# Performance work log

Hardware: AMD Instinct MI355X
Metric: run time of the kernel (lower is better)

Reference implementation:

```python
import jax, jax.numpy as jnp
import numpy as np

K = 4096          # num_embeddings
D = 256           # embedding_dim
BETA = 0.25
DECAY = 0.99
EPS = 1e-05

def setup_inputs() -> dict:
    key = jax.random.key(0)
    k1, k2, k3 = jax.random.split(key, 3)
    N = 65536
    return {
        "z": jax.random.normal(k1, (N, D), dtype=jnp.float32),
        "weight": jax.random.normal(k2, (K, D), dtype=jnp.float32),
        "ema_w": jax.random.normal(k3, (K, D), dtype=jnp.float32),
        "ema_cluster_size": jnp.ones((K,), dtype=jnp.float32),
    }

def reference(z, weight, ema_w, ema_cluster_size):
    # pairwise squared distances: [N, K]
    d = (jnp.sum(z * z, axis=1, keepdims=True)
         + jnp.sum(weight * weight, axis=1)
         - 2.0 * jnp.matmul(z, weight.T))
    idx = jnp.argmin(d, axis=1)                     # [N]
    encodings = jax.nn.one_hot(idx, K, dtype=z.dtype)  # [N, K]

    # EMA codebook update (training branch). In torch the results are re-wrapped
    # into fresh nn.Parameters, which detaches them from the autograd graph.
    def _ema(z_, enc_, ema_w_, cs_):
        cs = cs_ * DECAY + (1.0 - DECAY) * jnp.sum(enc_, axis=0)
        n = jnp.sum(cs)
        cs = (cs + EPS) / (n + K * EPS) * n
        dw = jnp.matmul(enc_.T, z_)                 # [K, D] scatter-add of z by code
        new_ema_w = ema_w_ * DECAY + (1.0 - DECAY) * dw
        new_weight = new_ema_w / cs[:, None]
        return cs, new_ema_w, new_weight
    new_cs, new_ema_w, new_weight = jax.lax.stop_gradient(
        _ema(z, encodings, ema_w, ema_cluster_size))

    z_q = new_weight[idx]                           # [N, D] gather from updated codebook
    loss = (jnp.mean((jax.lax.stop_gradient(z_q) - z) ** 2)
            + BETA * jnp.mean((z_q - jax.lax.stop_gradient(z)) ** 2))
    avg_probs = jnp.mean(encodings, axis=0)
    perplexity = jnp.exp(-jnp.sum(avg_probs * jnp.log(avg_probs + 1e-10)))
    z_q = z + jax.lax.stop_gradient(z_q - z)        # straight-through estimator
    return (z_q, idx[:, None], loss, perplexity, new_cs, new_ema_w, new_weight)
```

## Files before the change

### kernel.cpp

```cpp
#include <hip/hip_runtime.h>
#include <math.h>

#define NPTS 65536
#define DIMD 256
#define KCB  4096
#define MARGIN 2.0f

#define O_ZQ   0
#define O_IDX  16777216
#define O_LOSS 16842752
#define O_PERP 16842753
#define O_CS   16842754
#define O_EMAW 16846850
#define O_W    17895426

#define OFF_WSW   8388608
#define OFF_CCNT  8912896
#define OFF_CIDS  8978432
#define OFF_OFFS  10027008
#define OFF_CUR   10031232
#define OFF_ROWS  10035328
#define OFF_GMIN  10100864
#define OFF_CHOF  10166400
#define OFF_BMIN  10240000
#define OFF_RL    11288576
#define OFF_TPRE  12338176

#define CHK 64
#define MAXCHUNKS 5120
#define PADL 65600

#define RING 6
#define PFD  4

typedef __attribute__((ext_vector_type(8))) short short8;
typedef __attribute__((ext_vector_type(4))) float f32x4;

__device__ __forceinline__ unsigned short f2bf(float f) {
    unsigned u = __float_as_uint(f);
    return (unsigned short)((u + 0x7FFF + ((u >> 16) & 1)) >> 16);
}
__device__ __forceinline__ unsigned encf(float f) {
    unsigned u = __float_as_uint(f);
    return (u >> 31) ? ~u : (u | 0x80000000u);
}
__device__ __forceinline__ float decf(unsigned e) {
    unsigned u = (e & 0x80000000u) ? (e & 0x7fffffffu) : ~e;
    return __uint_as_float(u);
}

__global__ void k_prepz(const float* __restrict__ src, unsigned* __restrict__ dst,
                        float* __restrict__ ss) {
    int l   = threadIdx.x & 63;
    int row = blockIdx.x * 4 + (threadIdx.x >> 6);
    float4 v = ((const float4*)(src + (size_t)row * DIMD))[l];
    uint2 pk = make_uint2(f2bf(v.x) | (f2bf(v.y) << 16),
                          f2bf(v.z) | (f2bf(v.w) << 16));
    ((uint2*)dst)[(size_t)row * 64 + l] = pk;
    float s = v.x*v.x + v.y*v.y + v.z*v.z + v.w*v.w;
    #pragma unroll
    for (int off = 32; off; off >>= 1) s += __shfl_down(s, off);
    if (l == 0) ss[row] = s;
}

__global__ void k_prepw(const float* __restrict__ src, unsigned* __restrict__ dst,
                        float* __restrict__ ss) {
    int l   = threadIdx.x & 63;
    int row = blockIdx.x * 4 + (threadIdx.x >> 6);
    float4 v = ((const float4*)(src + (size_t)row * DIMD))[l];
    uint2 pk = make_uint2(f2bf(v.x) | (f2bf(v.y) << 16),
                          f2bf(v.z) | (f2bf(v.w) << 16));
    int g = row >> 4, n16 = row & 15;
    int c = l >> 3, q = (l >> 1) & 3, half = l & 1;
    ((uint2*)dst)[g * 1024 + c * 128 + (q * 16 + n16) * 2 + half] = pk;
    float s = v.x*v.x + v.y*v.y + v.z*v.z + v.w*v.w;
    #pragma unroll
    for (int off = 32; off; off >>= 1) s += __shfl_down(s, off);
    if (l == 0) ss[row] = s;
}

__launch_bounds__(256, 2)
__global__ void k_pass0(const unsigned* __restrict__ zbf,
                        const uint4* __restrict__ wsw4,
                        const float* __restrict__ wwg,
                        unsigned* __restrict__ gmin,
                        float* __restrict__ bmin) {
    __shared__ __align__(16) char smem[RING * 8192];
    __shared__ float lds_ww[2048];
    const int t = threadIdx.x, wv = t >> 6, l = t & 63;
    const int q = l >> 4, n16 = l & 15;
    const int rb    = blockIdx.x >> 1;
    const int half  = blockIdx.x & 1;
    const int row0  = rb * 256 + wv * 64;
    const int g0    = half * 128;
    const int ph0   = (blockIdx.x * 48) & 127;

    union U { uint4 u; short8 s; } afr[4][8];
    #pragma unroll
    for (int s = 0; s < 4; ++s) {
        const char* zb = (const char*)zbf + ((size_t)(row0 + s * 16 + n16) << 9) + q * 16;
        #pragma unroll
        for (int c = 0; c < 8; ++c) afr[s][c].u = *(const uint4*)(zb + c * 64);
    }

    auto stage = [&](int buf, int g) {
        const int ga = (ph0 + g) & 127;
        const uint4* srcb = wsw4 + (size_t)(g0 + ga) * 512;
        #pragma unroll
        for (int j = 0; j < 2; ++j) {
            int rrow = j * 4 + wv;
            __builtin_amdgcn_global_load_lds(
                (const __attribute__((address_space(1))) unsigned*)(srcb + rrow * 64 + l),
                (__attribute__((address_space(3))) unsigned*)(&smem[buf * 8192 + rrow * 1024]),
                16, 0, 0);
        }
    };

    for (int i = t; i < 2048; i += 256) lds_ww[i] = wwg[g0 * 16 + i];
    #pragma unroll
    for (int g = 0; g < PFD; ++g) stage(g, g);
    __syncthreads();

    float minv[16], bm[16];
    #pragma unroll
    for (int i = 0; i < 16; ++i) { minv[i] = 3.0e38f; bm[i] = 3.0e38f; }

    int buf = 0, sbuf = PFD;
    #pragma unroll 1
    for (int g = 0; g < 128; ++g) {
        if (g < 128 - PFD) {
            stage(sbuf, g + PFD);
            sbuf = (sbuf == RING - 1) ? 0 : sbuf + 1;
            asm volatile("s_waitcnt vmcnt(8)" ::: "memory");
        } else {
            asm volatile("s_waitcnt vmcnt(0)" ::: "memory");
        }
        __builtin_amdgcn_s_barrier();
        const char* sbase = smem + buf * 8192;
        buf = (buf == RING - 1) ? 0 : buf + 1;
        const int ga = (ph0 + g) & 127;
        f32x4 acc[4];
        #pragma unroll
        for (int s = 0; s < 4; ++s) acc[s] = (f32x4){0.f, 0.f, 0.f, 0.f};
        __builtin_amdgcn_s_setprio(1);
        #pragma unroll
        for (int c = 0; c < 8; ++c) {
            U bf; bf.u = *(const uint4*)(sbase + c * 1024 + (l << 4));
            #pragma unroll
            for (int s = 0; s < 4; ++s)
                acc[s] = __builtin_amdgcn_mfma_f32_16x16x32_bf16(afr[s][c].s, bf.s, acc[s], 0, 0, 0);
        }
        __builtin_amdgcn_s_setprio(0);
        float wwv = lds_ww[ga * 16 + n16];
        #pragma unroll
        for (int s = 0; s < 4; ++s)
            #pragma unroll
            for (int r = 0; r < 4; ++r)
                bm[s*4+r] = fminf(bm[s*4+r], fmaf(-2.f, acc[s][r], wwv));
        if ((g & 15) == 15) {
            const int blk = (g0 + ((ph0 + (g & ~15)) & 127)) >> 4;
            #pragma unroll
            for (int i = 0; i < 16; ++i) {
                float m = bm[i];
                minv[i] = fminf(minv[i], m);
                #pragma unroll
                for (int msk = 1; msk < 16; msk <<= 1) m = fminf(m, __shfl_xor(m, msk));
                if (n16 == 0)
                    bmin[(size_t)(row0 + (i >> 2) * 16 + q * 4 + (i & 3)) * 16 + blk] = m;
                bm[i] = 3.0e38f;
            }
        }
    }

    #pragma unroll
    for (int i = 0; i < 16; ++i) {
        float m = minv[i];
        #pragma unroll
        for (int msk = 1; msk < 16; msk <<= 1) m = fminf(m, __shfl_xor(m, msk));
        if (n16 == 0)
            atomicMin(&gmin[row0 + (i >> 2) * 16 + q * 4 + (i & 3)], encf(m));
    }
}

__global__ void k_bsel(const unsigned* __restrict__ gmin,
                       const float* __restrict__ bmin,
                       int* __restrict__ bcnt, int* __restrict__ rlist) {
    __shared__ int lcnt[16], lbase[16], lcur[16];
    int t = threadIdx.x;
    if (t < 16) { lcnt[t] = 0; lcur[t] = 0; }
    __syncthreads();
    int row = blockIdx.x * 256 + t;
    float thr = decf(gmin[row]) + MARGIN;
    const float* bm = bmin + (size_t)row * 16;
    unsigned qual = 0;
    #pragma unroll
    for (int b = 0; b < 16; ++b)
        if (bm[b] <= thr) { qual |= (1u << b); atomicAdd(&lcnt[b], 1); }
    __syncthreads();
    if (t < 16) lbase[t] = atomicAdd(&bcnt[t], lcnt[t]);
    __syncthreads();
    #pragma unroll
    for (int b = 0; b < 16; ++b)
        if (qual & (1u << b)) {
            int p = atomicAdd(&lcur[b], 1);
            rlist[b * PADL + lbase[b] + p] = row;
        }
}

__global__ void k_btile(const int* __restrict__ bcnt, int* __restrict__ rlist,
                        int* __restrict__ tpre) {
    __shared__ int tb[16];
    int t = threadIdx.x;
    if (t < 16) tb[t] = (bcnt[t] + 63) >> 6;
    __syncthreads();
    int b = t >> 4, j = t & 15;
    int n = bcnt[b], e = tb[b] * 64;
    for (int i = n + j; i < e; i += 16) rlist[b * PADL + i] = -1;
    if (t == 0) {
        int s = 0;
        for (int b2 = 0; b2 < 16; ++b2) { tpre[b2] = s; s += tb[b2]; }
        tpre[16] = s;
    }
}

__launch_bounds__(256, 2)
__global__ void k_pass1(const unsigned* __restrict__ zbf,
                        const uint4* __restrict__ wsw4,
                        const float* __restrict__ wwg,
                        const unsigned* __restrict__ gmin,
                        const int* __restrict__ tpre,
                        const int* __restrict__ rlist,
                        int* __restrict__ ccnt,
                        int* __restrict__ cids) {
    const int t = threadIdx.x, wv = t >> 6, l = t & 63;
    const int q = l >> 4, n16 = l & 15;
    const int ntiles = tpre[16];
    for (int tile = blockIdx.x * 4 + wv; tile < ntiles; tile += 2048) {
        int b = 0;
        while (b < 15 && tpre[b + 1] <= tile) ++b;
        const int* rl = rlist + b * PADL + (tile - tpre[b]) * 64;

        union U { uint4 u; short8 s; } afr[4][8];
        #pragma unroll
        for (int s = 0; s < 4; ++s) {
            int r = rl[s * 16 + n16];
            int rr = r < 0 ? 0 : r;
            const char* zb = (const char*)zbf + ((size_t)rr << 9) + q * 16;
            #pragma unroll
            for (int c = 0; c < 8; ++c) afr[s][c].u = *(const uint4*)(zb + c * 64);
        }
        float thr[16];
        #pragma unroll
        for (int i = 0; i < 16; ++i) {
            int r = rl[(i >> 2) * 16 + q * 4 + (i & 3)];
            thr[i] = (r < 0) ? -3.0e38f : decf(gmin[r]) + MARGIN;
        }

        #pragma unroll 2
        for (int g = 0; g < 16; ++g) {
            const int gg = b * 16 + g;
            const uint4* wp = wsw4 + (size_t)gg * 512 + l;
            f32x4 acc[4];
            #pragma unroll
            for (int s = 0; s < 4; ++s) acc[s] = (f32x4){0.f, 0.f, 0.f, 0.f};
            #pragma unroll
            for (int c = 0; c < 8; ++c) {
                U bf; bf.u = wp[c * 64];
                #pragma unroll
                for (int s = 0; s < 4; ++s)
                    acc[s] = __builtin_amdgcn_mfma_f32_16x16x32_bf16(afr[s][c].s, bf.s, acc[s], 0, 0, 0);
            }
            float wwv = wwg[gg * 16 + n16];
            #pragma unroll
            for (int s = 0; s < 4; ++s)
                #pragma unroll
                for (int r = 0; r < 4; ++r) {
                    float core = fmaf(-2.f, acc[s][r], wwv);
                    if (core <= thr[s*4+r]) {
                        int row = rl[s * 16 + q * 4 + r];
                        int pos = atomicAdd(&ccnt[row], 1);
                        if (pos < 16) cids[row * 16 + pos] = gg * 16 + n16;
                    }
                }
        }
    }
}

__global__ void k_refine(const float* __restrict__ z,
                         const float* __restrict__ w,
                         const float* __restrict__ zz,
                         const float* __restrict__ wwg,
                         const int* __restrict__ ccnt,
                         const int* __restrict__ cids,
                         float* __restrict__ counts,
                         int*   __restrict__ idxi,
                         float* __restrict__ idxf) {
    int l   = threadIdx.x & 63;
    int row = blockIdx.x * 4 + (threadIdx.x >> 6);
    int n = ccnt[row]; if (n > 16) n = 16;
    float4 zv = ((const float4*)(z + (size_t)row * DIMD))[l];
    float zzv = zz[row];
    float bd = 3.0e38f; int bi = 0x7fffffff;
    for (int j = 0; j < n; ++j) {
        int k = cids[row * 16 + j];
        float4 wv = ((const float4*)(w + (size_t)k * DIMD))[l];
        float s = zv.x*wv.x + zv.y*wv.y + zv.z*wv.z + zv.w*wv.w;
        #pragma unroll
        for (int off = 32; off; off >>= 1) s += __shfl_xor(s, off);
        float d = (zzv + wwg[k]) - 2.0f * s;
        if (d < bd || (d == bd && k < bi)) { bd = d; bi = k; }
    }
    if (l == 0) {
        idxi[row] = bi;
        idxf[row] = (float)bi;
        atomicAdd(&counts[bi], 1.0f);
    }
}

__global__ void k_offsets(const float* __restrict__ counts,
                          int* __restrict__ offs, int* __restrict__ cursor,
                          int* __restrict__ choffs) {
    __shared__ int sc[1024];
    int t = threadIdx.x;
    int c[4]; int s = 0;
    #pragma unroll
    for (int i = 0; i < 4; ++i) { c[i] = (int)counts[t * 4 + i]; s += c[i]; }
    sc[t] = s;
    __syncthreads();
    for (int d = 1; d < 1024; d <<= 1) {
        int v = (t >= d) ? sc[t - d] : 0;
        __syncthreads();
        sc[t] += v;
        __syncthreads();
    }
    int o = sc[t] - s;
    #pragma unroll
    for (int i = 0; i < 4; ++i) { offs[t*4+i] = o; cursor[t*4+i] = o; o += c[i]; }
    if (t == 1023) offs[4096] = sc[1023];
    __syncthreads();

    int ch[4]; int s2 = 0;
    #pragma unroll
    for (int i = 0; i < 4; ++i) { ch[i] = (c[i] + CHK - 1) / CHK; s2 += ch[i]; }
    sc[t] = s2;
    __syncthreads();
    for (int d = 1; d < 1024; d <<= 1) {
        int v = (t >= d) ? sc[t - d] : 0;
        __syncthreads();
        sc[t] += v;
        __syncthreads();
    }
    int o2 = sc[t] - s2;
    #pragma unroll
    for (int i = 0; i < 4; ++i) { choffs[t*4+i] = o2; o2 += ch[i]; }
    if (t == 1023) choffs[4096] = sc[1023];
}

__global__ void k_fill(const int* __restrict__ idxi, int* __restrict__ cursor,
                       int* __restrict__ rows) {
    int r = blockIdx.x * 256 + threadIdx.x;
    int k = idxi[r];
    int pos = atomicAdd(&cursor[k], 1);
    rows[pos] = r;
}

__global__ void k_dw(const float* __restrict__ z, const int* __restrict__ offs,
                     const int* __restrict__ choffs, const int* __restrict__ rows,
                     float* __restrict__ dw) {
    __shared__ float4 part[4][64];
    int b = blockIdx.x;
    if (b >= choffs[KCB]) return;
    int lo = 0, hi = KCB;
    while (hi - lo > 1) { int mid = (lo + hi) >> 1; if (choffs[mid] <= b) lo = mid; else hi = mid; }
    int k  = lo;
    int ci = b - choffs[k];
    int o0 = offs[k] + ci * CHK;
    int o1 = offs[k + 1]; if (o1 > o0 + CHK) o1 = o0 + CHK;
    int l = threadIdx.x & 63, j = threadIdx.x >> 6;
    float4 a = make_float4(0.f, 0.f, 0.f, 0.f);
    for (int i = o0 + j; i < o1; i += 4) {
        int r = rows[i];
        float4 v = ((const float4*)(z + (size_t)r * DIMD))[l];
        a.x += v.x; a.y += v.y; a.z += v.z; a.w += v.w;
    }
    part[j][l] = a;
    __syncthreads();
    if (j == 0) {
        float4 bb = part[0][l], c = part[1][l], d = part[2][l], e = part[3][l];
        a = make_float4(bb.x+c.x+d.x+e.x, bb.y+c.y+d.y+e.y,
                        bb.z+c.z+d.z+e.z, bb.w+c.w+d.w+e.w);
        float* p = dw + (size_t)k * DIMD + l * 4;
        if (choffs[k + 1] - choffs[k] == 1) {
            *(float4*)p = a;
        } else {
            atomicAdd(p + 0, a.x); atomicAdd(p + 1, a.y);
            atomicAdd(p + 2, a.z); atomicAdd(p + 3, a.w);
        }
    }
}

__global__ void k_cs(const float* __restrict__ ema_cs,
                     float* __restrict__ cs_io,
                     float* __restrict__ perp) {
    __shared__ float2 red[16];
    int t = threadIdx.x;
    float csd[4];
    float nl = 0.f, el = 0.f;
    #pragma unroll
    for (int i = 0; i < 4; ++i) {
        int k = t * 4 + i;
        float c  = cs_io[k];
        float cd = ema_cs[k] * 0.99f + 0.01f * c;
        csd[i] = cd;
        nl += cd;
        float p = c * (1.0f / 65536.0f);
        el += p * logf(p + 1e-10f);
    }
    #pragma unroll
    for (int off = 32; off; off >>= 1) { nl += __shfl_down(nl, off); el += __shfl_down(el, off); }
    if ((t & 63) == 0) red[t >> 6] = make_float2(nl, el);
    __syncthreads();
    if (t == 0) {
        float n = 0.f, e = 0.f;
        for (int i = 0; i < 16; ++i) { n += red[i].x; e += red[i].y; }
        red[0] = make_float2(n, e);
        perp[0] = expf(-e);
    }
    __syncthreads();
    float n = red[0].x;
    float scale = n / (n + 4096.0f * 1e-5f);
    #pragma unroll
    for (int i = 0; i < 4; ++i)
        cs_io[t * 4 + i] = (csd[i] + 1e-5f) * scale;
}

__global__ void k_emaw(const float* __restrict__ ema_w,
                       const float* __restrict__ cs,
                       float* __restrict__ emaw_io,
                       float* __restrict__ wout) {
    int i = (blockIdx.x * 256 + threadIdx.x) * 4;
    int k = i >> 8;
    float4 dv = *(const float4*)(emaw_io + i);
    float4 ev = *(const float4*)(ema_w + i);
    float c = cs[k];
    float4 ne;
    ne.x = ev.x * 0.99f + 0.01f * dv.x;
    ne.y = ev.y * 0.99f + 0.01f * dv.y;
    ne.z = ev.z * 0.99f + 0.01f * dv.z;
    ne.w = ev.w * 0.99f + 0.01f * dv.w;
    *(float4*)(emaw_io + i) = ne;
    float4 nw = make_float4(ne.x / c, ne.y / c, ne.z / c, ne.w / c);
    *(float4*)(wout + i) = nw;
}

__global__ void k_zq(const float* __restrict__ z,
                     const float* __restrict__ wnew,
                     const int* __restrict__ idxi,
                     float* __restrict__ zq,
                     float* __restrict__ sqacc) {
    __shared__ float red[4];
    int i = (blockIdx.x * 256 + threadIdx.x) * 4;
    int n = i >> 8;
    int d = i & 255;
    int k = idxi[n];
    float4 wv = *(const float4*)(wnew + (k << 8) + d);
    float4 zv = *(const float4*)(z + i);
    float4 o;
    o.x = zv.x + (wv.x - zv.x);
    o.y = zv.y + (wv.y - zv.y);
    o.z = zv.z + (wv.z - zv.z);
    o.w = zv.w + (wv.w - zv.w);
    *(float4*)(zq + i) = o;
    float dx = wv.x - zv.x, dy = wv.y - zv.y, dz = wv.z - zv.z, dw_ = wv.w - zv.w;
    float s = dx*dx + dy*dy + dz*dz + dw_*dw_;
    #pragma unroll
    for (int off = 32; off; off >>= 1) s += __shfl_down(s, off);
    int lane = threadIdx.x & 63;
    if (lane == 0) red[threadIdx.x >> 6] = s;
    __syncthreads();
    if (threadIdx.x == 0)
        atomicAdd(&sqacc[blockIdx.x & 255], red[0] + red[1] + red[2] + red[3]);
}

__global__ void k_final(const float* __restrict__ sqacc, float* __restrict__ loss) {
    __shared__ float red[4];
    int t = threadIdx.x;
    float s = sqacc[t];
    #pragma unroll
    for (int off = 32; off; off >>= 1) s += __shfl_down(s, off);
    if ((t & 63) == 0) red[t >> 6] = s;
    __syncthreads();
    if (t == 0)
        loss[0] = 1.25f * (red[0] + red[1] + red[2] + red[3]) * (1.0f / 16777216.0f);
}

extern "C" void kernel_launch(void* const* d_in, const int* in_sizes, int n_in,
                              void* d_out, int out_size, void* d_ws, size_t ws_size,
                              hipStream_t stream) {
    const float* z      = (const float*)d_in[0];
    const float* weight = (const float*)d_in[1];
    const float* ema_w  = (const float*)d_in[2];
    const float* ema_cs = (const float*)d_in[3];
    float* out = (float*)d_out;
    float* ws  = (float*)d_ws;

    int*   bcnt = (int*)ws;
    float* scal = ws + 4096;
    int*   idxi = (int*)(ws + 8192);

    unsigned* zbf    = (unsigned*)(out + O_ZQ);
    uint4*    wsw4   = (uint4*)(out + O_ZQ + OFF_WSW);
    int*      ccnt   = (int*)(out + O_ZQ + OFF_CCNT);
    int*      cids   = (int*)(out + O_ZQ + OFF_CIDS);
    int*      offs   = (int*)(out + O_ZQ + OFF_OFFS);
    int*      cursor = (int*)(out + O_ZQ + OFF_CUR);
    int*      rows   = (int*)(out + O_ZQ + OFF_ROWS);
    unsigned* gmin   = (unsigned*)(out + O_ZQ + OFF_GMIN);
    int*      choffs = (int*)(out + O_ZQ + OFF_CHOF);
    float*    bmin   = out + O_ZQ + OFF_BMIN;
    int*      rlist  = (int*)(out + O_ZQ + OFF_RL);
    int*      tpre   = (int*)(out + O_ZQ + OFF_TPRE);
    float*    zz     = out + O_EMAW;
    float*    wwg    = out + O_EMAW + 65536;

    hipMemsetAsync(bcnt,       0,    16 * 4, stream);
    hipMemsetAsync(scal,       0,    256 * 4, stream);
    hipMemsetAsync(out + O_CS, 0,    (size_t)KCB * 4, stream);
    hipMemsetAsync(ccnt,       0,    (size_t)NPTS * 4, stream);
    hipMemsetAsync(gmin,       0xFF, (size_t)NPTS * 4, stream);

    k_prepz  <<<NPTS / 4, 256, 0, stream>>>(z, zbf, zz);
    k_prepw  <<<KCB  / 4, 256, 0, stream>>>(weight, (unsigned*)wsw4, wwg);
    k_pass0  <<<512, 256, 0, stream>>>(zbf, wsw4, wwg, gmin, bmin);
    k_bsel   <<<NPTS / 256, 256, 0, stream>>>(gmin, bmin, bcnt, rlist);
    k_btile  <<<1, 256, 0, stream>>>(bcnt, rlist, tpre);
    k_pass1  <<<512, 256, 0, stream>>>(zbf, wsw4, wwg, gmin, tpre, rlist,
                                       ccnt, cids);
    k_refine <<<NPTS / 4, 256, 0, stream>>>(z, weight, zz, wwg, ccnt, cids,
                                            out + O_CS, idxi, out + O_IDX);
    hipMemsetAsync(out + O_EMAW, 0, (size_t)KCB * DIMD * 4, stream);
    k_offsets<<<1, 1024, 0, stream>>>(out + O_CS, offs, cursor, choffs);
    k_fill   <<<NPTS / 256, 256, 0, stream>>>(idxi, cursor, rows);
    k_cs     <<<1, 1024, 0, stream>>>(ema_cs, out + O_CS, out + O_PERP);
    k_dw     <<<MAXCHUNKS, 256, 0, stream>>>(z, offs, choffs, rows, out + O_EMAW);
    k_emaw   <<<(KCB * DIMD) / 1024, 256, 0, stream>>>(ema_w, out + O_CS,
                                                       out + O_EMAW, out + O_W);
    k_zq     <<<(NPTS * DIMD) / 1024, 256, 0, stream>>>(z, out + O_W, idxi,
                                                        out + O_ZQ, scal);
    k_final  <<<1, 256, 0, stream>>>(scal, out + O_LOSS);
}
```

Before: 494.9 us.

## Fuse prep kernels, fold memsets into kernels, merge count stages, widen pass0 staging

```diff
diff --git a/kernel.cpp b/kernel.cpp
--- a/kernel.cpp
+++ b/kernel.cpp
@@ -24,14 +24,13 @@
 #define OFF_CHOF  10166400
 #define OFF_BMIN  10240000
 #define OFF_RL    11288576
-#define OFF_TPRE  12338176
 
 #define CHK 64
 #define MAXCHUNKS 5120
 #define PADL 65600
 
-#define RING 6
-#define PFD  4
+#define RING0 4
+#define NSLOT 64
 
 typedef __attribute__((ext_vector_type(8))) short short8;
 typedef __attribute__((ext_vector_type(4))) float f32x4;
@@ -49,34 +48,42 @@
     return __uint_as_float(u);
 }
 
-__global__ void k_prepz(const float* __restrict__ src, unsigned* __restrict__ dst,
-                        float* __restrict__ ss) {
-    int l   = threadIdx.x & 63;
-    int row = blockIdx.x * 4 + (threadIdx.x >> 6);
-    float4 v = ((const float4*)(src + (size_t)row * DIMD))[l];
-    uint2 pk = make_uint2(f2bf(v.x) | (f2bf(v.y) << 16),
-                          f2bf(v.z) | (f2bf(v.w) << 16));
-    ((uint2*)dst)[(size_t)row * 64 + l] = pk;
-    float s = v.x*v.x + v.y*v.y + v.z*v.z + v.w*v.w;
-    #pragma unroll
-    for (int off = 32; off; off >>= 1) s += __shfl_down(s, off);
-    if (l == 0) ss[row] = s;
-}
-
-__global__ void k_prepw(const float* __restrict__ src, unsigned* __restrict__ dst,
-                        float* __restrict__ ss) {
-    int l   = threadIdx.x & 63;
-    int row = blockIdx.x * 4 + (threadIdx.x >> 6);
-    float4 v = ((const float4*)(src + (size_t)row * DIMD))[l];
-    uint2 pk = make_uint2(f2bf(v.x) | (f2bf(v.y) << 16),
-                          f2bf(v.z) | (f2bf(v.w) << 16));
-    int g = row >> 4, n16 = row & 15;
-    int c = l >> 3, q = (l >> 1) & 3, half = l & 1;
-    ((uint2*)dst)[g * 1024 + c * 128 + (q * 16 + n16) * 2 + half] = pk;
-    float s = v.x*v.x + v.y*v.y + v.z*v.z + v.w*v.w;
-    #pragma unroll
-    for (int off = 32; off; off >>= 1) s += __shfl_down(s, off);
-    if (l == 0) ss[row] = s;
+__global__ void k_prep(const float* __restrict__ zsrc, const float* __restrict__ wsrc,
+                       unsigned* __restrict__ zdst, unsigned* __restrict__ wdst,
+                       float* __restrict__ zz, float* __restrict__ wwg,
+                       unsigned* __restrict__ gmin, int* __restrict__ ccnt,
+                       float* __restrict__ cs, float* __restrict__ scal,
+                       int* __restrict__ bcnt) {
+    int b = blockIdx.x, t = threadIdx.x;
+    int l = t & 63;
+    if (b < NPTS / 4) {
+        int row = b * 4 + (t >> 6);
+        float4 v = ((const float4*)(zsrc + (size_t)row * DIMD))[l];
+        uint2 pk = make_uint2(f2bf(v.x) | (f2bf(v.y) << 16),
+                              f2bf(v.z) | (f2bf(v.w) << 16));
+        ((uint2*)zdst)[(size_t)row * 64 + l] = pk;
+        float s = v.x*v.x + v.y*v.y + v.z*v.z + v.w*v.w;
+        #pragma unroll
+        for (int off = 32; off; off >>= 1) s += __shfl_down(s, off);
+        if (l == 0) zz[row] = s;
+        if (t < 4) gmin[b * 4 + t] = 0xFFFFFFFFu;
+        else if (t < 8) ccnt[b * 4 + (t - 4)] = 0;
+    } else {
+        int b2 = b - NPTS / 4;
+        int row = b2 * 4 + (t >> 6);
+        float4 v = ((const float4*)(wsrc + (size_t)row * DIMD))[l];
+        uint2 pk = make_uint2(f2bf(v.x) | (f2bf(v.y) << 16),
+                              f2bf(v.z) | (f2bf(v.w) << 16));
+        int g = row >> 4, n16 = row & 15;
+        int c = l >> 3, q = (l >> 1) & 3, half = l & 1;
+        ((uint2*)wdst)[g * 1024 + c * 128 + (q * 16 + n16) * 2 + half] = pk;
+        float s = v.x*v.x + v.y*v.y + v.z*v.z + v.w*v.w;
+        #pragma unroll
+        for (int off = 32; off; off >>= 1) s += __shfl_down(s, off);
+        if (l == 0) wwg[row] = s;
+        if (t < 4) cs[b2 * 4 + t] = 0.f;
+        if (b2 == 0) { scal[t] = 0.f; if (t < 16) bcnt[t] = 0; }
+    }
 }
 
 __launch_bounds__(256, 2)
@@ -85,7 +92,7 @@
                         const float* __restrict__ wwg,
                         unsigned* __restrict__ gmin,
                         float* __restrict__ bmin) {
-    __shared__ __align__(16) char smem[RING * 8192];
+    __shared__ __align__(16) char smem[RING0 * 16384];
     __shared__ float lds_ww[2048];
     const int t = threadIdx.x, wv = t >> 6, l = t & 63;
     const int q = l >> 4, n16 = l & 15;
@@ -93,7 +100,7 @@
     const int half  = blockIdx.x & 1;
     const int row0  = rb * 256 + wv * 64;
     const int g0    = half * 128;
-    const int ph0   = (blockIdx.x * 48) & 127;
+    const int ph0s  = ((blockIdx.x * 3) & 7) * 8;
 
     union U { uint4 u; short8 s; } afr[4][8];
     #pragma unroll
@@ -103,62 +110,65 @@
         for (int c = 0; c < 8; ++c) afr[s][c].u = *(const uint4*)(zb + c * 64);
     }
 
-    auto stage = [&](int buf, int g) {
-        const int ga = (ph0 + g) & 127;
-        const uint4* srcb = wsw4 + (size_t)(g0 + ga) * 512;
-        #pragma unroll
-        for (int j = 0; j < 2; ++j) {
+    auto stage = [&](int buf, int s) {
+        const int sa = (ph0s + s) & 63;
+        const uint4* srcb = wsw4 + (size_t)(g0 + sa * 2) * 512;
+        #pragma unroll
+        for (int j = 0; j < 4; ++j) {
             int rrow = j * 4 + wv;
             __builtin_amdgcn_global_load_lds(
                 (const __attribute__((address_space(1))) unsigned*)(srcb + rrow * 64 + l),
-                (__attribute__((address_space(3))) unsigned*)(&smem[buf * 8192 + rrow * 1024]),
+                (__attribute__((address_space(3))) unsigned*)(&smem[buf * 16384 + rrow * 1024]),
                 16, 0, 0);
         }
     };
 
     for (int i = t; i < 2048; i += 256) lds_ww[i] = wwg[g0 * 16 + i];
-    #pragma unroll
-    for (int g = 0; g < PFD; ++g) stage(g, g);
+    stage(0, 0);
+    stage(1, 1);
     __syncthreads();
 
     float minv[16], bm[16];
     #pragma unroll
     for (int i = 0; i < 16; ++i) { minv[i] = 3.0e38f; bm[i] = 3.0e38f; }
 
-    int buf = 0, sbuf = PFD;
+    int buf = 0, sbuf = 2;
     #pragma unroll 1
-    for (int g = 0; g < 128; ++g) {
-        if (g < 128 - PFD) {
-            stage(sbuf, g + PFD);
-            sbuf = (sbuf == RING - 1) ? 0 : sbuf + 1;
+    for (int s = 0; s < NSLOT; ++s) {
+        if (s < NSLOT - 2) {
+            stage(sbuf, s + 2);
+            sbuf = (sbuf + 1) & 3;
             asm volatile("s_waitcnt vmcnt(8)" ::: "memory");
         } else {
             asm volatile("s_waitcnt vmcnt(0)" ::: "memory");
         }
         __builtin_amdgcn_s_barrier();
-        const char* sbase = smem + buf * 8192;
-        buf = (buf == RING - 1) ? 0 : buf + 1;
-        const int ga = (ph0 + g) & 127;
-        f32x4 acc[4];
-        #pragma unroll
-        for (int s = 0; s < 4; ++s) acc[s] = (f32x4){0.f, 0.f, 0.f, 0.f};
-        __builtin_amdgcn_s_setprio(1);
-        #pragma unroll
-        for (int c = 0; c < 8; ++c) {
-            U bf; bf.u = *(const uint4*)(sbase + c * 1024 + (l << 4));
-            #pragma unroll
-            for (int s = 0; s < 4; ++s)
-                acc[s] = __builtin_amdgcn_mfma_f32_16x16x32_bf16(afr[s][c].s, bf.s, acc[s], 0, 0, 0);
-        }
-        __builtin_amdgcn_s_setprio(0);
-        float wwv = lds_ww[ga * 16 + n16];
-        #pragma unroll
-        for (int s = 0; s < 4; ++s)
-            #pragma unroll
-            for (int r = 0; r < 4; ++r)
-                bm[s*4+r] = fminf(bm[s*4+r], fmaf(-2.f, acc[s][r], wwv));
-        if ((g & 15) == 15) {
-            const int blk = (g0 + ((ph0 + (g & ~15)) & 127)) >> 4;
+        const char* sbase = smem + buf * 16384;
+        buf = (buf + 1) & 3;
+        const int sa = (ph0s + s) & 63;
+        #pragma unroll
+        for (int g2 = 0; g2 < 2; ++g2) {
+            f32x4 acc[4];
+            #pragma unroll
+            for (int s4 = 0; s4 < 4; ++s4) acc[s4] = (f32x4){0.f, 0.f, 0.f, 0.f};
+            __builtin_amdgcn_s_setprio(1);
+            #pragma unroll
+            for (int c = 0; c < 8; ++c) {
+                U bf; bf.u = *(const uint4*)(sbase + g2 * 8192 + c * 1024 + (l << 4));
+                #pragma unroll
+                for (int s4 = 0; s4 < 4; ++s4)
+                    acc[s4] = __builtin_amdgcn_mfma_f32_16x16x32_bf16(afr[s4][c].s, bf.s, acc[s4], 0, 0, 0);
+            }
+            __builtin_amdgcn_s_setprio(0);
+            float wwv = lds_ww[(sa * 2 + g2) * 16 + n16];
+            #pragma unroll
+            for (int s4 = 0; s4 < 4; ++s4)
+                #pragma unroll
+                for (int r = 0; r < 4; ++r)
+                    bm[s4*4+r] = fminf(bm[s4*4+r], fmaf(-2.f, acc[s4][r], wwv));
+        }
+        if ((s & 7) == 7) {
+            const int blk = (g0 >> 4) + (((ph0s + (s & ~7)) & 63) >> 3);
             #pragma unroll
             for (int i = 0; i < 16; ++i) {
                 float m = bm[i];
@@ -207,53 +217,52 @@
         }
 }
 
-__global__ void k_btile(const int* __restrict__ bcnt, int* __restrict__ rlist,
-                        int* __restrict__ tpre) {
-    __shared__ int tb[16];
-    int t = threadIdx.x;
-    if (t < 16) tb[t] = (bcnt[t] + 63) >> 6;
-    __syncthreads();
-    int b = t >> 4, j = t & 15;
-    int n = bcnt[b], e = tb[b] * 64;
-    for (int i = n + j; i < e; i += 16) rlist[b * PADL + i] = -1;
-    if (t == 0) {
-        int s = 0;
-        for (int b2 = 0; b2 < 16; ++b2) { tpre[b2] = s; s += tb[b2]; }
-        tpre[16] = s;
-    }
-}
-
 __launch_bounds__(256, 2)
 __global__ void k_pass1(const unsigned* __restrict__ zbf,
                         const uint4* __restrict__ wsw4,
                         const float* __restrict__ wwg,
                         const unsigned* __restrict__ gmin,
-                        const int* __restrict__ tpre,
+                        const int* __restrict__ bcnt,
                         const int* __restrict__ rlist,
                         int* __restrict__ ccnt,
                         int* __restrict__ cids) {
     const int t = threadIdx.x, wv = t >> 6, l = t & 63;
     const int q = l >> 4, n16 = l & 15;
-    const int ntiles = tpre[16];
+    int bc[16];
+    #pragma unroll
+    for (int i = 0; i < 16; ++i) bc[i] = bcnt[i];
+    int tp[17]; tp[0] = 0;
+    #pragma unroll
+    for (int i = 0; i < 16; ++i) tp[i + 1] = tp[i] + ((bc[i] + 63) >> 6);
+    const int ntiles = tp[16];
+
     for (int tile = blockIdx.x * 4 + wv; tile < ntiles; tile += 2048) {
-        int b = 0;
-        while (b < 15 && tpre[b + 1] <= tile) ++b;
-        const int* rl = rlist + b * PADL + (tile - tpre[b]) * 64;
+        int b = 0, tpb = 0, nb = bc[0];
+        #pragma unroll
+        for (int i = 1; i < 16; ++i)
+            if (tp[i] <= tile) { b = i; tpb = tp[i]; nb = bc[i]; }
+        const int lim = nb - (tile - tpb) * 64;
+        const int* rl = rlist + b * PADL + (tile - tpb) * 64;
 
         union U { uint4 u; short8 s; } afr[4][8];
         #pragma unroll
         for (int s = 0; s < 4; ++s) {
-            int r = rl[s * 16 + n16];
+            int idx = s * 16 + n16;
+            int r = (idx < lim) ? rl[idx] : -1;
             int rr = r < 0 ? 0 : r;
             const char* zb = (const char*)zbf + ((size_t)rr << 9) + q * 16;
             #pragma unroll
             for (int c = 0; c < 8; ++c) afr[s][c].u = *(const uint4*)(zb + c * 64);
         }
+        int rowid[16];
         float thr[16];
         #pragma unroll
         for (int i = 0; i < 16; ++i) {
-            int r = rl[(i >> 2) * 16 + q * 4 + (i & 3)];
-            thr[i] = (r < 0) ? -3.0e38f : decf(gmin[r]) + MARGIN;
+            int idx = (i >> 2) * 16 + q * 4 + (i & 3);
+            int r = (idx < lim) ? rl[idx] : -1;
+            rowid[i] = r;
+            thr[i] = -3.0e38f;
+            if (r >= 0) thr[i] = decf(gmin[r]) + MARGIN;
         }
 
         #pragma unroll 2
@@ -277,7 +286,7 @@
                 for (int r = 0; r < 4; ++r) {
                     float core = fmaf(-2.f, acc[s][r], wwv);
                     if (core <= thr[s*4+r]) {
-                        int row = rl[s * 16 + q * 4 + r];
+                        int row = rowid[s * 4 + r];
                         int pos = atomicAdd(&ccnt[row], 1);
                         if (pos < 16) cids[row * 16 + pos] = gg * 16 + n16;
                     }
@@ -317,10 +326,13 @@
     }
 }
 
-__global__ void k_offsets(const float* __restrict__ counts,
-                          int* __restrict__ offs, int* __restrict__ cursor,
-                          int* __restrict__ choffs) {
+__global__ void k_mid(const float* __restrict__ counts,
+                      const float* __restrict__ ema_cs,
+                      int* __restrict__ offs, int* __restrict__ cursor,
+                      int* __restrict__ choffs,
+                      float* __restrict__ cs_io, float* __restrict__ perp) {
     __shared__ int sc[1024];
+    __shared__ float2 redf[16];
     int t = threadIdx.x;
     int c[4]; int s = 0;
     #pragma unroll
@@ -354,11 +366,42 @@
     #pragma unroll
     for (int i = 0; i < 4; ++i) { choffs[t*4+i] = o2; o2 += ch[i]; }
     if (t == 1023) choffs[4096] = sc[1023];
+    __syncthreads();
+
+    float csd[4]; float nl = 0.f, el = 0.f;
+    #pragma unroll
+    for (int i = 0; i < 4; ++i) {
+        float cf = (float)c[i];
+        float cd = ema_cs[t * 4 + i] * 0.99f + 0.01f * cf;
+        csd[i] = cd;
+        nl += cd;
+        float p = cf * (1.0f / 65536.0f);
+        el += p * logf(p + 1e-10f);
+    }
+    #pragma unroll
+    for (int off = 32; off; off >>= 1) { nl += __shfl_down(nl, off); el += __shfl_down(el, off); }
+    if ((t & 63) == 0) redf[t >> 6] = make_float2(nl, el);
+    __syncthreads();
+    if (t == 0) {
+        float n = 0.f, e = 0.f;
+        for (int i = 0; i < 16; ++i) { n += redf[i].x; e += redf[i].y; }
+        redf[0] = make_float2(n, e);
+        perp[0] = expf(-e);
+    }
+    __syncthreads();
+    float n = redf[0].x;
+    float scale = n / (n + 4096.0f * 1e-5f);
+    #pragma unroll
+    for (int i = 0; i < 4; ++i)
+        cs_io[t * 4 + i] = (csd[i] + 1e-5f) * scale;
 }
 
 __global__ void k_fill(const int* __restrict__ idxi, int* __restrict__ cursor,
-                       int* __restrict__ rows) {
+                       int* __restrict__ rows, float* __restrict__ dw) {
     int r = blockIdx.x * 256 + threadIdx.x;
+    float4* p = (float4*)(dw + (size_t)r * 16);
+    float4 zf = make_float4(0.f, 0.f, 0.f, 0.f);
+    p[0] = zf; p[1] = zf; p[2] = zf; p[3] = zf;
     int k = idxi[r];
     int pos = atomicAdd(&cursor[k], 1);
     rows[pos] = r;
@@ -397,41 +440,6 @@
             atomicAdd(p + 2, a.z); atomicAdd(p + 3, a.w);
         }
     }
-}
-
-__global__ void k_cs(const float* __restrict__ ema_cs,
-                     float* __restrict__ cs_io,
-                     float* __restrict__ perp) {
-    __shared__ float2 red[16];
-    int t = threadIdx.x;
-    float csd[4];
-    float nl = 0.f, el = 0.f;
-    #pragma unroll
-    for (int i = 0; i < 4; ++i) {
-        int k = t * 4 + i;
-        float c  = cs_io[k];
-        float cd = ema_cs[k] * 0.99f + 0.01f * c;
-        csd[i] = cd;
-        nl += cd;
-        float p = c * (1.0f / 65536.0f);
-        el += p * logf(p + 1e-10f);
-    }
-    #pragma unroll
-    for (int off = 32; off; off >>= 1) { nl += __shfl_down(nl, off); el += __shfl_down(el, off); }
-    if ((t & 63) == 0) red[t >> 6] = make_float2(nl, el);
-    __syncthreads();
-    if (t == 0) {
-        float n = 0.f, e = 0.f;
-        for (int i = 0; i < 16; ++i) { n += red[i].x; e += red[i].y; }
-        red[0] = make_float2(n, e);
-        perp[0] = expf(-e);
-    }
-    __syncthreads();
-    float n = red[0].x;
-    float scale = n / (n + 4096.0f * 1e-5f);
-    #pragma unroll
-    for (int i = 0; i < 4; ++i)
-        cs_io[t * 4 + i] = (csd[i] + 1e-5f) * scale;
 }
 
 __global__ void k_emaw(const float* __restrict__ ema_w,
@@ -519,29 +527,22 @@
     int*      choffs = (int*)(out + O_ZQ + OFF_CHOF);
     float*    bmin   = out + O_ZQ + OFF_BMIN;
     int*      rlist  = (int*)(out + O_ZQ + OFF_RL);
-    int*      tpre   = (int*)(out + O_ZQ + OFF_TPRE);
     float*    zz     = out + O_EMAW;
     float*    wwg    = out + O_EMAW + 65536;
 
-    hipMemsetAsync(bcnt,       0,    16 * 4, stream);
-    hipMemsetAsync(scal,       0,    256 * 4, stream);
-    hipMemsetAsync(out + O_CS, 0,    (size_t)KCB * 4, stream);
-    hipMemsetAsync(ccnt,       0,    (size_t)NPTS * 4, stream);
-    hipMemsetAsync(gmin,       0xFF, (size_t)NPTS * 4, stream);
-
-    k_prepz  <<<NPTS / 4, 256, 0, stream>>>(z, zbf, zz);
-    k_prepw  <<<KCB  / 4, 256, 0, stream>>>(weight, (unsigned*)wsw4, wwg);
+    k_prep   <<<NPTS / 4 + KCB / 4, 256, 0, stream>>>(z, weight, zbf,
+                                                      (unsigned*)wsw4, zz, wwg,
+                                                      gmin, ccnt, out + O_CS,
+                                                      scal, bcnt);
     k_pass0  <<<512, 256, 0, stream>>>(zbf, wsw4, wwg, gmin, bmin);
     k_bsel   <<<NPTS / 256, 256, 0, stream>>>(gmin, bmin, bcnt, rlist);
-    k_btile  <<<1, 256, 0, stream>>>(bcnt, rlist, tpre);
-    k_pass1  <<<512, 256, 0, stream>>>(zbf, wsw4, wwg, gmin, tpre, rlist,
+    k_pass1  <<<512, 256, 0, stream>>>(zbf, wsw4, wwg, gmin, bcnt, rlist,
                                        ccnt, cids);
     k_refine <<<NPTS / 4, 256, 0, stream>>>(z, weight, zz, wwg, ccnt, cids,
                                             out + O_CS, idxi, out + O_IDX);
-    hipMemsetAsync(out + O_EMAW, 0, (size_t)KCB * DIMD * 4, stream);
-    k_offsets<<<1, 1024, 0, stream>>>(out + O_CS, offs, cursor, choffs);
-    k_fill   <<<NPTS / 256, 256, 0, stream>>>(idxi, cursor, rows);
-    k_cs     <<<1, 1024, 0, stream>>>(ema_cs, out + O_CS, out + O_PERP);
+    k_mid    <<<1, 1024, 0, stream>>>(out + O_CS, ema_cs, offs, cursor, choffs,
+                                      out + O_CS, out + O_PERP);
+    k_fill   <<<NPTS / 256, 256, 0, stream>>>(idxi, cursor, rows, out + O_EMAW);
     k_dw     <<<MAXCHUNKS, 256, 0, stream>>>(z, offs, choffs, rows, out + O_EMAW);
     k_emaw   <<<(KCB * DIMD) / 1024, 256, 0, stream>>>(ema_w, out + O_CS,
                                                        out + O_EMAW, out + O_W);
```

Result: faster. 441.2 us (-10.9%).
